# Kernel optimization log

Measured on AMD Instinct MI355X. Metric: run time of the kernel, lower is better.

The kernel has to match this reference:

```python
import jax, jax.numpy as jnp
import numpy as np

HIDDEN = 768
N_HEADS = 12
D_HEAD = 64
B, T = 4, 2048


def setup_inputs() -> dict:
    key = jax.random.key(0)
    ks = jax.random.split(key, 5)
    s = 0.02
    return {
        "x": jax.random.normal(ks[0], (B, T, HIDDEN), dtype=jnp.float32),
        "w_q": jax.random.normal(ks[1], (HIDDEN, HIDDEN), dtype=jnp.float32) * s,
        "w_k": jax.random.normal(ks[2], (HIDDEN, HIDDEN), dtype=jnp.float32) * s,
        "w_v": jax.random.normal(ks[3], (HIDDEN, HIDDEN), dtype=jnp.float32) * s,
        "w_o": jax.random.normal(ks[4], (HIDDEN, HIDDEN), dtype=jnp.float32) * s,
    }


def reference(x, w_q, w_k, w_v, w_o):
    # nn.Linear applies x @ W^T; weights here are [out, in] like torch.
    b, t, h = x.shape
    q = (x @ w_q.T).reshape(b, t, N_HEADS, D_HEAD)
    k = (x @ w_k.T).reshape(b, t, N_HEADS, D_HEAD)
    v = (x @ w_v.T).reshape(b, t, N_HEADS, D_HEAD)
    # scores: [b, heads, t, t]
    scores = jnp.einsum("bqhd,bkhd->bhqk", q, k) / jnp.sqrt(jnp.float32(D_HEAD))
    weights = jax.nn.softmax(scores, axis=-1)
    # dropout p=0.0 -> identity
    ctx = jnp.einsum("bhqk,bkhd->bqhd", weights, v).reshape(b, t, h)
    return ctx @ w_o.T
```

## Files before the change

### kernel.cpp

```cpp
#include <hip/hip_runtime.h>

#define HIDDEN 768
#define NH 12
#define DH 64
#define BB 4
#define TT 2048
#define MTOT (BB * TT)

typedef __bf16 bf16x8 __attribute__((ext_vector_type(8)));
typedef short s16x8 __attribute__((ext_vector_type(8)));
typedef float f32x4 __attribute__((ext_vector_type(4)));

__device__ __forceinline__ unsigned short f2b(float f) {
    unsigned u = __builtin_bit_cast(unsigned, f);
    u += 0x7fffu + ((u >> 16) & 1u);
    return (unsigned short)(u >> 16);
}

__device__ __forceinline__ unsigned pack_bf16(float a, float b) {
    return __builtin_amdgcn_perm(__builtin_bit_cast(unsigned, b),
                                 __builtin_bit_cast(unsigned, a), 0x07060302u);
}

typedef const __attribute__((address_space(1))) unsigned int* gas_ptr;
typedef __attribute__((address_space(3))) unsigned int* las_ptr;
__device__ __forceinline__ void gload16(const void* g, void* l) {
    __builtin_amdgcn_global_load_lds((gas_ptr)(uintptr_t)g, (las_ptr)(uintptr_t)l, 16, 0, 0);
}

__global__ __launch_bounds__(256) void cvt_all(const float* __restrict__ x,
                                               const float* __restrict__ wq,
                                               const float* __restrict__ wk,
                                               const float* __restrict__ wv,
                                               const float* __restrict__ wo,
                                               unsigned short* __restrict__ out) {
    const size_t NX8 = (size_t)MTOT * HIDDEN / 8;
    const size_t NW8 = (size_t)HIDDEN * HIDDEN / 8;
    size_t i = (size_t)blockIdx.x * 256 + threadIdx.x;
    const float* src;
    size_t off = i;
    float scale = 1.0f;
    if (i < NX8) { src = x; }
    else if (i < NX8 + NW8) { src = wq; off = i - NX8; scale = 0.18033688011112042f; }
    else if (i < NX8 + 2 * NW8) { src = wk; off = i - NX8 - NW8; }
    else if (i < NX8 + 3 * NW8) { src = wv; off = i - NX8 - 2 * NW8; }
    else { src = wo; off = i - NX8 - 3 * NW8; }
    const float4* p = (const float4*)src + off * 2;
    float4 a = p[0], b = p[1];
    union { uint4 u; unsigned short s[8]; } t;
    t.s[0] = f2b(a.x * scale); t.s[1] = f2b(a.y * scale);
    t.s[2] = f2b(a.z * scale); t.s[3] = f2b(a.w * scale);
    t.s[4] = f2b(b.x * scale); t.s[5] = f2b(b.y * scale);
    t.s[6] = f2b(b.z * scale); t.s[7] = f2b(b.w * scale);
    ((uint4*)out)[i] = t.u;
}

template <int MODE>
__device__ __forceinline__ void gemm_body(const unsigned short* __restrict__ A,
                                          const unsigned short* __restrict__ Bm,
                                          float* __restrict__ Cf,
                                          unsigned short* __restrict__ Cb,
                                          int mBase, int nBase, int N) {
    __shared__ __align__(16) unsigned short Al[2][128][64];
    __shared__ __align__(16) unsigned short Bl[2][128][64];
    const int tid = threadIdx.x;
    const int lane = tid & 63;
    const int wave = tid >> 6;
    const int quad = lane >> 4;
    const int l16 = lane & 15;
    const int mw = (wave >> 1) * 64;
    const int nw = (wave & 1) * 64;
    const int srow = wave * 32 + (lane >> 3);
    const int swiz = ((lane & 7) ^ (lane >> 3)) * 8;
    const unsigned short* Asrc = A + (size_t)(mBase + srow) * HIDDEN + swiz;
    const unsigned short* Bsrc = Bm + (size_t)(nBase + srow) * HIDDEN + swiz;

    f32x4 acc[4][4];
#pragma unroll
    for (int mt = 0; mt < 4; ++mt)
#pragma unroll
        for (int nt = 0; nt < 4; ++nt) acc[mt][nt] = (f32x4){0.f, 0.f, 0.f, 0.f};

    auto stage = [&](int buf, int kb) {
#pragma unroll
        for (int i = 0; i < 4; ++i) {
            gload16(Asrc + (size_t)i * 8 * HIDDEN + kb * 64, &Al[buf][wave * 32 + i * 8][0]);
            gload16(Bsrc + (size_t)i * 8 * HIDDEN + kb * 64, &Bl[buf][wave * 32 + i * 8][0]);
        }
    };

    stage(0, 0);
    for (int kb = 0; kb < HIDDEN / 64; ++kb) {
        __syncthreads();
        if (kb + 1 < HIDDEN / 64) stage((kb + 1) & 1, kb + 1);
        const int buf = kb & 1;
#pragma unroll
        for (int ks = 0; ks < 2; ++ks) {
            const int cc = ((ks * 4 + quad) ^ (l16 & 7)) * 8;
            bf16x8 af[4], bf[4];
#pragma unroll
            for (int t = 0; t < 4; ++t) {
                af[t] = *(const bf16x8*)&Al[buf][mw + t * 16 + l16][cc];
                bf[t] = *(const bf16x8*)&Bl[buf][nw + t * 16 + l16][cc];
            }
#pragma unroll
            for (int mt = 0; mt < 4; ++mt)
#pragma unroll
                for (int nt = 0; nt < 4; ++nt)
                    acc[mt][nt] = __builtin_amdgcn_mfma_f32_16x16x32_bf16(
                        af[mt], bf[nt], acc[mt][nt], 0, 0, 0);
        }
    }

#pragma unroll
    for (int mt = 0; mt < 4; ++mt)
#pragma unroll
        for (int nt = 0; nt < 4; ++nt) {
            if (MODE == 2) {
                ushort4 h;
                h.x = f2b(acc[mt][nt][0]); h.y = f2b(acc[mt][nt][1]);
                h.z = f2b(acc[mt][nt][2]); h.w = f2b(acc[mt][nt][3]);
                int m0 = mBase + mw + mt * 16 + quad * 4;
                int col = nBase + nw + nt * 16 + l16;
                *(ushort4*)&Cb[(size_t)col * MTOT + m0] = h;
            } else {
#pragma unroll
                for (int r = 0; r < 4; ++r) {
                    int row = mBase + mw + mt * 16 + quad * 4 + r;
                    int col = nBase + nw + nt * 16 + l16;
                    float v = acc[mt][nt][r];
                    if (MODE == 1)
                        Cf[(size_t)row * N + col] = v;
                    else
                        Cb[(size_t)row * N + col] = f2b(v);
                }
            }
        }
}

__global__ __launch_bounds__(256) void gemm_qkv(const unsigned short* __restrict__ A,
                                                const unsigned short* __restrict__ W0,
                                                unsigned short* __restrict__ C0,
                                                unsigned short* __restrict__ VT) {
    const int wsel = blockIdx.x / 6;
    const int nb = blockIdx.x % 6;
    if (wsel < 2)
        gemm_body<0>(A, W0 + (size_t)wsel * HIDDEN * HIDDEN, nullptr,
                     C0 + (size_t)wsel * MTOT * HIDDEN, blockIdx.y * 128, nb * 128, HIDDEN);
    else
        gemm_body<2>(A, W0 + 2 * (size_t)HIDDEN * HIDDEN, nullptr, VT,
                     blockIdx.y * 128, nb * 128, HIDDEN);
}

__global__ __launch_bounds__(256) void gemm_out(const unsigned short* __restrict__ A,
                                                const unsigned short* __restrict__ Bm,
                                                float* __restrict__ Cf) {
    gemm_body<1>(A, Bm, Cf, nullptr, blockIdx.y * 128, blockIdx.x * 128, HIDDEN);
}

__global__ __launch_bounds__(256) void attn_kernel(const unsigned short* __restrict__ Qg,
                                                   const unsigned short* __restrict__ Kg,
                                                   const unsigned short* __restrict__ VTg,
                                                   unsigned short* __restrict__ Ctx) {
    __shared__ __align__(16) unsigned short Kl[2][64][64];
    __shared__ __align__(16) unsigned short Vl[2][64][64];
    __shared__ __align__(16) unsigned int Pl[4][32][36];
    const int tid = threadIdx.x;
    const int lane = tid & 63;
    const int wave = tid >> 6;
    const int quad = lane >> 4;
    const int l16 = lane & 15;
    const int qt = blockIdx.x;
    const int bh = blockIdx.y;
    const int b = bh / NH, h = bh % NH;
    const int qrow0 = b * TT + qt * 128;
    const int col0 = h * DH;

    const int srow = wave * 16 + (lane >> 3);
    const int swiz = ((lane & 7) ^ (lane >> 3)) * 8;
    const unsigned short* Ksrc = Kg + (size_t)(b * TT + srow) * HIDDEN + col0 + swiz;
    const unsigned short* Vsrc = VTg + (size_t)(col0 + srow) * MTOT + b * TT + swiz;

    auto stage = [&](int buf, int kt) {
#pragma unroll
        for (int i = 0; i < 2; ++i) {
            gload16(Ksrc + (size_t)(kt * 64 + i * 8) * HIDDEN, &Kl[buf][wave * 16 + i * 8][0]);
            gload16(Vsrc + (size_t)(i * 8) * MTOT + kt * 64, &Vl[buf][wave * 16 + i * 8][0]);
        }
    };

    bf16x8 qf[2][2];
#pragma unroll
    for (int mt = 0; mt < 2; ++mt)
#pragma unroll
        for (int ks = 0; ks < 2; ++ks)
            qf[mt][ks] = *(const bf16x8*)&Qg[(size_t)(qrow0 + wave * 32 + mt * 16 + l16) * HIDDEN +
                                             col0 + ks * 32 + quad * 8];

    s16x8 osv;
#pragma unroll
    for (int e = 0; e < 8; ++e) osv[e] = 0x3F80;
    const bf16x8 ones = __builtin_bit_cast(bf16x8, osv);

    f32x4 o[2][4];
    f32x4 lacc[2];
#pragma unroll
    for (int mt = 0; mt < 2; ++mt) {
        lacc[mt] = (f32x4){0.f, 0.f, 0.f, 0.f};
#pragma unroll
        for (int nt = 0; nt < 4; ++nt) o[mt][nt] = (f32x4){0.f, 0.f, 0.f, 0.f};
    }

    stage(0, 0);
    for (int kt = 0; kt < TT / 64; ++kt) {
        __syncthreads();
        if (kt + 1 < TT / 64) stage((kt + 1) & 1, kt + 1);
        const int buf = kt & 1;

        f32x4 s[2][4];
#pragma unroll
        for (int mt = 0; mt < 2; ++mt)
#pragma unroll
            for (int nt = 0; nt < 4; ++nt) s[mt][nt] = (f32x4){0.f, 0.f, 0.f, 0.f};
#pragma unroll
        for (int ks = 0; ks < 2; ++ks) {
            const int cc = ((ks * 4 + quad) ^ (l16 & 7)) * 8;
            bf16x8 kf[4];
#pragma unroll
            for (int nt = 0; nt < 4; ++nt)
                kf[nt] = *(const bf16x8*)&Kl[buf][nt * 16 + l16][cc];
#pragma unroll
            for (int mt = 0; mt < 2; ++mt)
#pragma unroll
                for (int nt = 0; nt < 4; ++nt)
                    s[mt][nt] = __builtin_amdgcn_mfma_f32_16x16x32_bf16(kf[nt], qf[mt][ks],
                                                                        s[mt][nt], 0, 0, 0);
        }

#pragma unroll
        for (int mt = 0; mt < 2; ++mt) {
            const int row = mt * 16 + l16;
#pragma unroll
            for (int nt = 0; nt < 4; ++nt) {
                float p0 = __builtin_amdgcn_exp2f(s[mt][nt][0]);
                float p1 = __builtin_amdgcn_exp2f(s[mt][nt][1]);
                float p2 = __builtin_amdgcn_exp2f(s[mt][nt][2]);
                float p3 = __builtin_amdgcn_exp2f(s[mt][nt][3]);
                uint2 w;
                w.x = pack_bf16(p0, p1);
                w.y = pack_bf16(p2, p3);
                *(uint2*)&Pl[wave][row][nt * 8 + quad * 2] = w;
            }
        }

#pragma unroll
        for (int ks = 0; ks < 2; ++ks) {
            const int cc = ((ks * 4 + quad) ^ (l16 & 7)) * 8;
            bf16x8 pf[2], vf[4];
#pragma unroll
            for (int mt = 0; mt < 2; ++mt)
                pf[mt] = *(const bf16x8*)((const unsigned short*)&Pl[wave][mt * 16 + l16][0] +
                                          ks * 32 + quad * 8);
#pragma unroll
            for (int nt = 0; nt < 4; ++nt)
                vf[nt] = *(const bf16x8*)&Vl[buf][nt * 16 + l16][cc];
#pragma unroll
            for (int mt = 0; mt < 2; ++mt)
                lacc[mt] = __builtin_amdgcn_mfma_f32_16x16x32_bf16(pf[mt], ones, lacc[mt], 0, 0, 0);
#pragma unroll
            for (int mt = 0; mt < 2; ++mt)
#pragma unroll
                for (int nt = 0; nt < 4; ++nt)
                    o[mt][nt] = __builtin_amdgcn_mfma_f32_16x16x32_bf16(pf[mt], vf[nt],
                                                                        o[mt][nt], 0, 0, 0);
        }
    }

#pragma unroll
    for (int mt = 0; mt < 2; ++mt)
#pragma unroll
        for (int r = 0; r < 4; ++r) {
            float inv = __builtin_amdgcn_rcpf(lacc[mt][r]);
            int row = qrow0 + wave * 32 + mt * 16 + quad * 4 + r;
#pragma unroll
            for (int nt = 0; nt < 4; ++nt)
                Ctx[(size_t)row * HIDDEN + col0 + nt * 16 + l16] = f2b(o[mt][nt][r] * inv);
        }
}

extern "C" void kernel_launch(void* const* d_in, const int* in_sizes, int n_in,
                              void* d_out, int out_size, void* d_ws, size_t ws_size,
                              hipStream_t stream) {
    const float* x = (const float*)d_in[0];
    const float* wq = (const float*)d_in[1];
    const float* wk = (const float*)d_in[2];
    const float* wv = (const float*)d_in[3];
    const float* wo = (const float*)d_in[4];
    float* out = (float*)d_out;

    const size_t NX = (size_t)MTOT * HIDDEN;
    const size_t NW = (size_t)HIDDEN * HIDDEN;
    unsigned short* ws = (unsigned short*)d_ws;
    unsigned short* xb = ws;
    unsigned short* wqb = xb + NX;
    unsigned short* wob = wqb + 3 * NW;
    unsigned short* qb = wob + NW;
    unsigned short* kb = qb + NX;
    unsigned short* cb = kb + NX;
    unsigned short* vtb = cb + NX;

    cvt_all<<<(int)((NX + 4 * NW) / 8 / 256), 256, 0, stream>>>(x, wq, wk, wv, wo, xb);

    gemm_qkv<<<dim3(18, MTOT / 128), 256, 0, stream>>>(xb, wqb, qb, vtb);

    attn_kernel<<<dim3(TT / 128, BB * NH), 256, 0, stream>>>(qb, kb, vtb, cb);

    gemm_out<<<dim3(6, MTOT / 128), 256, 0, stream>>>(cb, wob, out);
}
```

Baseline: 222.3 us.

## Single-buffer GEMM LDS, add occupancy hints, and halve output GEMM M-tile

Drops the LDS double buffer in the shared GEMM body, so each k-step loads and then syncs before computing. This cuts LDS per block from 64KB to 32KB or less, which should let more blocks sit on a CU, and the kernels now request 4 blocks per CU. The output projection GEMM uses 64-row M tiles so the grid doubles to 768 blocks for better CU fill. The cost is that global loads no longer overlap MFMA work within a block, so latency hiding now depends on occupancy across blocks.

```diff
diff --git a/kernel.cpp b/kernel.cpp
--- a/kernel.cpp
+++ b/kernel.cpp
@@ -55,56 +55,55 @@
     ((uint4*)out)[i] = t.u;
 }
 
-template <int MODE>
+template <int MODE, int MROWS>
 __device__ __forceinline__ void gemm_body(const unsigned short* __restrict__ A,
                                           const unsigned short* __restrict__ Bm,
                                           float* __restrict__ Cf,
                                           unsigned short* __restrict__ Cb,
                                           int mBase, int nBase, int N) {
-    __shared__ __align__(16) unsigned short Al[2][128][64];
-    __shared__ __align__(16) unsigned short Bl[2][128][64];
+    __shared__ __align__(16) unsigned short Al[MROWS][64];
+    __shared__ __align__(16) unsigned short Bl[128][64];
+    const int MT = MROWS / 32;
     const int tid = threadIdx.x;
     const int lane = tid & 63;
     const int wave = tid >> 6;
     const int quad = lane >> 4;
     const int l16 = lane & 15;
-    const int mw = (wave >> 1) * 64;
+    const int mw = (wave >> 1) * (MROWS / 2);
     const int nw = (wave & 1) * 64;
-    const int srow = wave * 32 + (lane >> 3);
-    const int swiz = ((lane & 7) ^ (lane >> 3)) * 8;
-    const unsigned short* Asrc = A + (size_t)(mBase + srow) * HIDDEN + swiz;
-    const unsigned short* Bsrc = Bm + (size_t)(nBase + srow) * HIDDEN + swiz;
-
-    f32x4 acc[4][4];
-#pragma unroll
-    for (int mt = 0; mt < 4; ++mt)
+    const int r8 = lane >> 3;
+    const int swiz = ((lane & 7) ^ r8) * 8;
+    const unsigned short* Asrc = A + (size_t)(mBase + wave * (MROWS / 4) + r8) * HIDDEN + swiz;
+    const unsigned short* Bsrc = Bm + (size_t)(nBase + wave * 32 + r8) * HIDDEN + swiz;
+
+    f32x4 acc[MT][4];
+#pragma unroll
+    for (int mt = 0; mt < MT; ++mt)
 #pragma unroll
         for (int nt = 0; nt < 4; ++nt) acc[mt][nt] = (f32x4){0.f, 0.f, 0.f, 0.f};
 
-    auto stage = [&](int buf, int kb) {
-#pragma unroll
-        for (int i = 0; i < 4; ++i) {
-            gload16(Asrc + (size_t)i * 8 * HIDDEN + kb * 64, &Al[buf][wave * 32 + i * 8][0]);
-            gload16(Bsrc + (size_t)i * 8 * HIDDEN + kb * 64, &Bl[buf][wave * 32 + i * 8][0]);
-        }
-    };
-
-    stage(0, 0);
     for (int kb = 0; kb < HIDDEN / 64; ++kb) {
+        if (kb) __syncthreads();
+#pragma unroll
+        for (int i = 0; i < MROWS / 32; ++i)
+            gload16(Asrc + (size_t)i * 8 * HIDDEN + kb * 64,
+                    &Al[wave * (MROWS / 4) + i * 8][0]);
+#pragma unroll
+        for (int j = 0; j < 4; ++j)
+            gload16(Bsrc + (size_t)j * 8 * HIDDEN + kb * 64, &Bl[wave * 32 + j * 8][0]);
         __syncthreads();
-        if (kb + 1 < HIDDEN / 64) stage((kb + 1) & 1, kb + 1);
-        const int buf = kb & 1;
 #pragma unroll
         for (int ks = 0; ks < 2; ++ks) {
             const int cc = ((ks * 4 + quad) ^ (l16 & 7)) * 8;
-            bf16x8 af[4], bf[4];
-#pragma unroll
-            for (int t = 0; t < 4; ++t) {
-                af[t] = *(const bf16x8*)&Al[buf][mw + t * 16 + l16][cc];
-                bf[t] = *(const bf16x8*)&Bl[buf][nw + t * 16 + l16][cc];
-            }
-#pragma unroll
-            for (int mt = 0; mt < 4; ++mt)
+            bf16x8 af[MT], bf[4];
+#pragma unroll
+            for (int mt = 0; mt < MT; ++mt)
+                af[mt] = *(const bf16x8*)&Al[mw + mt * 16 + l16][cc];
+#pragma unroll
+            for (int nt = 0; nt < 4; ++nt)
+                bf[nt] = *(const bf16x8*)&Bl[nw + nt * 16 + l16][cc];
+#pragma unroll
+            for (int mt = 0; mt < MT; ++mt)
 #pragma unroll
                 for (int nt = 0; nt < 4; ++nt)
                     acc[mt][nt] = __builtin_amdgcn_mfma_f32_16x16x32_bf16(
@@ -113,7 +112,7 @@
     }
 
 #pragma unroll
-    for (int mt = 0; mt < 4; ++mt)
+    for (int mt = 0; mt < MT; ++mt)
 #pragma unroll
         for (int nt = 0; nt < 4; ++nt) {
             if (MODE == 2) {
@@ -138,24 +137,24 @@
         }
 }
 
-__global__ __launch_bounds__(256) void gemm_qkv(const unsigned short* __restrict__ A,
-                                                const unsigned short* __restrict__ W0,
-                                                unsigned short* __restrict__ C0,
-                                                unsigned short* __restrict__ VT) {
+__global__ __launch_bounds__(256, 4) void gemm_qkv(const unsigned short* __restrict__ A,
+                                                   const unsigned short* __restrict__ W0,
+                                                   unsigned short* __restrict__ C0,
+                                                   unsigned short* __restrict__ VT) {
     const int wsel = blockIdx.x / 6;
     const int nb = blockIdx.x % 6;
     if (wsel < 2)
-        gemm_body<0>(A, W0 + (size_t)wsel * HIDDEN * HIDDEN, nullptr,
-                     C0 + (size_t)wsel * MTOT * HIDDEN, blockIdx.y * 128, nb * 128, HIDDEN);
+        gemm_body<0, 128>(A, W0 + (size_t)wsel * HIDDEN * HIDDEN, nullptr,
+                          C0 + (size_t)wsel * MTOT * HIDDEN, blockIdx.y * 128, nb * 128, HIDDEN);
     else
-        gemm_body<2>(A, W0 + 2 * (size_t)HIDDEN * HIDDEN, nullptr, VT,
-                     blockIdx.y * 128, nb * 128, HIDDEN);
-}
-
-__global__ __launch_bounds__(256) void gemm_out(const unsigned short* __restrict__ A,
-                                                const unsigned short* __restrict__ Bm,
-                                                float* __restrict__ Cf) {
-    gemm_body<1>(A, Bm, Cf, nullptr, blockIdx.y * 128, blockIdx.x * 128, HIDDEN);
+        gemm_body<2, 128>(A, W0 + 2 * (size_t)HIDDEN * HIDDEN, nullptr, VT,
+                          blockIdx.y * 128, nb * 128, HIDDEN);
+}
+
+__global__ __launch_bounds__(256, 4) void gemm_out(const unsigned short* __restrict__ A,
+                                                   const unsigned short* __restrict__ Bm,
+                                                   float* __restrict__ Cf) {
+    gemm_body<1, 64>(A, Bm, Cf, nullptr, blockIdx.y * 64, blockIdx.x * 128, HIDDEN);
 }
 
 __global__ __launch_bounds__(256) void attn_kernel(const unsigned short* __restrict__ Qg,
@@ -315,5 +314,5 @@
 
     attn_kernel<<<dim3(TT / 128, BB * NH), 256, 0, stream>>>(qb, kb, vtb, cb);
 
-    gemm_out<<<dim3(6, MTOT / 128), 256, 0, stream>>>(cb, wob, out);
-}
+    gemm_out<<<dim3(6, MTOT / 64), 256, 0, stream>>>(cb, wob, out);
+}
```

After: 220.5 us. About the same (-0.8%).
